# Kernel tuning notes

Hardware: AMD Instinct MI355X
Metric: run time of the kernel (lower is better)

The kernel has to match this reference:

```python
import jax, jax.numpy as jnp
import numpy as np

ROPE_BASE = 10000.0

def _rms_norm(x):
    eps = jnp.asarray(jnp.finfo(x.dtype).eps, x.dtype)
    return x * jax.lax.rsqrt(jnp.mean(x * x, axis=-1, keepdims=True) + eps)

def _rope(x):
    # x: [B, S, H, hd]; rotate-halves variant: y1 = x1*cos + x2*sin, y2 = -x1*sin + x2*cos
    S, hd = x.shape[1], x.shape[3]
    d = hd // 2
    inv_freq = 1.0 / (ROPE_BASE ** (jnp.arange(0, hd, 2, dtype=jnp.float32) / hd))  # [d]
    t = jnp.arange(S, dtype=jnp.float32)
    freqs = jnp.outer(t, inv_freq)                       # [S, d]
    cos = jnp.cos(freqs)[None, :, None, :].astype(x.dtype)
    sin = jnp.sin(freqs)[None, :, None, :].astype(x.dtype)
    x1, x2 = x[..., :d], x[..., d:]
    return jnp.concatenate([x1 * cos + x2 * sin, -x1 * sin + x2 * cos], axis=-1)

def setup_inputs() -> dict:
    key = jax.random.key(0)
    ks = jax.random.split(key, 7)
    B, S, D = 1, 2048, 1024
    std = 0.02
    return {
        "x": jax.random.normal(ks[0], (B, S, D), jnp.float32),
        "v1": jax.random.normal(ks[1], (B, S, D), jnp.float32),
        "Wq": jax.random.normal(ks[2], (D, D), jnp.float32) * std,
        "Wk": jax.random.normal(ks[3], (D, D), jnp.float32) * std,
        "Wv": jax.random.normal(ks[4], (D, D), jnp.float32) * std,
        "Wout": jax.random.normal(ks[5], (D, D), jnp.float32) * std,
        "lambdas": jnp.float32(0.5),
        "n_heads": 16,
    }

def reference(x, v1, Wq, Wk, Wv, Wout, lambdas, n_heads):
    B, S, D = x.shape
    H = n_heads
    hd = D // H
    # QKV projections (CastedLinear, no bias)
    q = (x @ Wq.T).reshape(B, S, H, hd)
    k = (x @ Wk.T).reshape(B, S, H, hd)
    v = (x @ Wv.T).reshape(B, S, H, hd)
    # value residual mix with first-layer values v1
    v = (1.0 - lambdas) * v + lambdas * v1.reshape(B, S, H, hd)
    # per-head RMS norm (no learned scale) then RoPE
    q, k = _rms_norm(q), _rms_norm(k)
    q, k = _rope(q), _rope(k)
    # causal attention (flex_attention default: softmax, scale 1/sqrt(hd))
    scale = 1.0 / jnp.sqrt(jnp.asarray(hd, x.dtype))
    scores = jnp.einsum('bqhd,bkhd->bhqk', q, k) * scale        # [B,H,S,S]
    causal = jnp.tril(jnp.ones((S, S), dtype=bool))
    scores = jnp.where(causal[None, None], scores, jnp.asarray(-jnp.inf, scores.dtype))
    p = jax.nn.softmax(scores, axis=-1)
    y = jnp.einsum('bhqk,bkhd->bqhd', p, v).reshape(B, S, D)
    y = y @ Wout.T
    return (y, v1)
```

## Files before the change

kernel.cpp:

```cpp
#include <hip/hip_runtime.h>
#include <hip/hip_bf16.h>

#define S_LEN 2048
#define D_DIM 1024
#define NH    16
#define NEG_BIG (-1.0e30f)

#define EPI_NORMROPE   1
#define EPI_VMIX_T     2
#define EPI_F32        3
#define EPI_NORMROPE_Q 4
#define EPI_F32A       5

typedef __attribute__((ext_vector_type(8))) short bf16x8;
typedef __attribute__((ext_vector_type(4))) float f32x4;
typedef const __attribute__((address_space(1))) unsigned char gu8_t;
typedef __attribute__((address_space(3))) unsigned char lu8_t;

__device__ __forceinline__ float bf2f(unsigned short h) {
    union { unsigned int u; float f; } v; v.u = ((unsigned int)h) << 16; return v.f;
}
__device__ __forceinline__ unsigned short f2b(float f) {
    union { float f; unsigned int u; } v; v.f = f;
    unsigned int u = v.u;
    return (unsigned short)((u + 0x7FFFu + ((u >> 16) & 1u)) >> 16);
}
__device__ __forceinline__ unsigned short f2b_trunc(float f) {
    union { float f; unsigned int u; } v; v.f = f;
    return (unsigned short)(v.u >> 16);
}

__global__ __launch_bounds__(256)
void to_bf16(const float* __restrict__ x,  const float* __restrict__ wq,
             const float* __restrict__ wk, const float* __restrict__ wv,
             const float* __restrict__ wo,
             unsigned short* __restrict__ xb,  unsigned short* __restrict__ wqb,
             unsigned short* __restrict__ wkb, unsigned short* __restrict__ wvb,
             unsigned short* __restrict__ wob)
{
    const int z = blockIdx.y;
    const float* s; unsigned short* d; int n;
    switch (z) {
        case 0: s = x;  d = xb;  n = S_LEN * D_DIM; break;
        case 1: s = wq; d = wqb; n = D_DIM * D_DIM; break;
        case 2: s = wk; d = wkb; n = D_DIM * D_DIM; break;
        case 3: s = wv; d = wvb; n = D_DIM * D_DIM; break;
        default: s = wo; d = wob; n = D_DIM * D_DIM; break;
    }
    int i8 = blockIdx.x * 256 + threadIdx.x;
    if (i8 * 8 >= n) return;
    const float* sp = s + (size_t)i8 * 8;
    float4 lo = *(const float4*)sp, hi = *(const float4*)(sp + 4);
    uint4 p;
    p.x = f2b(lo.x) | ((unsigned)f2b(lo.y) << 16);
    p.y = f2b(lo.z) | ((unsigned)f2b(lo.w) << 16);
    p.z = f2b(hi.x) | ((unsigned)f2b(hi.y) << 16);
    p.w = f2b(hi.z) | ((unsigned)f2b(hi.w) << 16);
    *(uint4*)(d + (size_t)i8 * 8) = p;
}

__global__ __launch_bounds__(256, 3)
void gemm_bt(const unsigned short* __restrict__ A,
             const unsigned short* __restrict__ B0, const unsigned short* __restrict__ B1,
             const unsigned short* __restrict__ B2,
             void* __restrict__ C0, void* __restrict__ C1, void* __restrict__ C2,
             const float* __restrict__ vmix, const float* __restrict__ lam,
             int epiPack, int splitK)
{
    const int which = blockIdx.z;
    const unsigned short* Bp;
    void* C;
    int epi, kLo, kHi;
    if (splitK) {
        Bp = B0; C = C0; epi = epiPack & 0xff;
        kLo = which * (D_DIM / 2); kHi = kLo + D_DIM / 2;
    } else {
        Bp = (which == 0) ? B0 : ((which == 1) ? B1 : B2);
        C  = (which == 0) ? C0 : ((which == 1) ? C1 : C2);
        epi = (epiPack >> (8 * which)) & 0xff;
        kLo = 0; kHi = D_DIM;
    }
    const int tn = blockIdx.x * 128;
    const int tm = blockIdx.y * 128;

    __shared__ unsigned short Asl[128 * 32];
    __shared__ unsigned short Bsl[128 * 32];

    const int t    = threadIdx.x;
    const int lane = t & 63;
    const int wave = t >> 6;
    const int wm   = (wave >> 1) * 64;
    const int wn   = (wave & 1) * 64;
    const int lrow = lane & 15;
    const int quad = lane >> 4;
    const int srow = lane >> 2;
    const int scol = (lane & 3) * 8;

    f32x4 acc[4][4];
    #pragma unroll
    for (int i = 0; i < 4; ++i)
        #pragma unroll
        for (int j = 0; j < 4; ++j) {
            f32x4 z = {0.f, 0.f, 0.f, 0.f};
            acc[i][j] = z;
        }

    for (int k0 = kLo; k0 < kHi; k0 += 32) {
        #pragma unroll
        for (int rep = 0; rep < 2; ++rep) {
            int grp = wave * 2 + rep;
            int row = grp * 16 + srow;
            __builtin_amdgcn_global_load_lds(
                (gu8_t*)(A + (size_t)(tm + row) * D_DIM + k0 + scol),
                (lu8_t*)&Asl[grp * 512], 16, 0, 0);
            __builtin_amdgcn_global_load_lds(
                (gu8_t*)(Bp + (size_t)(tn + row) * D_DIM + k0 + scol),
                (lu8_t*)&Bsl[grp * 512], 16, 0, 0);
        }
        __syncthreads();
        bf16x8 af[4], bfr[4];
        #pragma unroll
        for (int i = 0; i < 4; ++i)
            af[i] = *(const bf16x8*)(&Asl[(wm + i * 16 + lrow) * 32 + quad * 8]);
        #pragma unroll
        for (int j = 0; j < 4; ++j)
            bfr[j] = *(const bf16x8*)(&Bsl[(wn + j * 16 + lrow) * 32 + quad * 8]);
        #pragma unroll
        for (int i = 0; i < 4; ++i)
            #pragma unroll
            for (int j = 0; j < 4; ++j)
                acc[i][j] = __builtin_amdgcn_mfma_f32_16x16x32_bf16(af[i], bfr[j], acc[i][j], 0, 0, 0);
        __syncthreads();
    }

    if (epi == EPI_NORMROPE || epi == EPI_NORMROPE_Q) {
        const float post = (epi == EPI_NORMROPE_Q) ? 0.18033688011112042f : 1.0f;
        #pragma unroll
        for (int i = 0; i < 4; ++i) {
            #pragma unroll
            for (int r = 0; r < 4; ++r) {
                int row = tm + wm + i * 16 + quad * 4 + r;
                float v0 = acc[i][0][r], v1 = acc[i][1][r];
                float v2 = acc[i][2][r], v3 = acc[i][3][r];
                float ss = v0 * v0 + v1 * v1 + v2 * v2 + v3 * v3;
                ss += __shfl_xor(ss, 1); ss += __shfl_xor(ss, 2);
                ss += __shfl_xor(ss, 4); ss += __shfl_xor(ss, 8);
                float rms = rsqrtf(ss * (1.f / 64.f) + 1.1920929e-7f) * post;
                v0 *= rms; v1 *= rms; v2 *= rms; v3 *= rms;
                float fs = (float)row;
                float a0 = fs * exp2f(-0.41524101186092030f * (float)lrow);
                float a1 = fs * exp2f(-0.41524101186092030f * (float)(16 + lrow));
                float s0, c0, s1, c1;
                __sincosf(a0, &s0, &c0);
                __sincosf(a1, &s1, &c1);
                unsigned short* Cb = (unsigned short*)C;
                size_t base = (size_t)row * D_DIM + tn + wn + lrow;
                Cb[base]      = f2b(v0 * c0 + v2 * s0);
                Cb[base + 16] = f2b(v1 * c1 + v3 * s1);
                Cb[base + 32] = f2b(-v0 * s0 + v2 * c0);
                Cb[base + 48] = f2b(-v1 * s1 + v3 * c1);
            }
        }
    } else if (epi == EPI_VMIX_T) {
        float lamf = *lam;
        #pragma unroll
        for (int i = 0; i < 4; ++i) {
            int cm0 = tm + wm + i * 16 + quad * 4;
            #pragma unroll
            for (int j = 0; j < 4; ++j) {
                int cn = tn + wn + j * 16 + lrow;
                ushort4 pk;
                float vals[4];
                #pragma unroll
                for (int r = 0; r < 4; ++r) {
                    size_t idx = (size_t)(cm0 + r) * D_DIM + cn;
                    vals[r] = (1.f - lamf) * acc[i][j][r] + lamf * vmix[idx];
                }
                pk.x = f2b(vals[0]); pk.y = f2b(vals[1]);
                pk.z = f2b(vals[2]); pk.w = f2b(vals[3]);
                *(ushort4*)((unsigned short*)C + (size_t)cn * S_LEN + cm0) = pk;
            }
        }
    } else if (epi == EPI_F32A) {
        #pragma unroll
        for (int i = 0; i < 4; ++i) {
            int cm0 = tm + wm + i * 16 + quad * 4;
            #pragma unroll
            for (int j = 0; j < 4; ++j) {
                int cn = tn + wn + j * 16 + lrow;
                #pragma unroll
                for (int r = 0; r < 4; ++r)
                    atomicAdd(&((float*)C)[(size_t)(cm0 + r) * D_DIM + cn], acc[i][j][r]);
            }
        }
    } else {
        #pragma unroll
        for (int i = 0; i < 4; ++i) {
            int cm0 = tm + wm + i * 16 + quad * 4;
            #pragma unroll
            for (int j = 0; j < 4; ++j) {
                int cn = tn + wn + j * 16 + lrow;
                #pragma unroll
                for (int r = 0; r < 4; ++r)
                    ((float*)C)[(size_t)(cm0 + r) * D_DIM + cn] = acc[i][j][r];
            }
        }
    }
}

__global__ __launch_bounds__(256, 3)
void attn_mfma(const unsigned short* Qb,
               const unsigned short* __restrict__ Kb,
               const unsigned short* __restrict__ Vtg,
               float* __restrict__ Opart, float* __restrict__ Lpart)
{
    const int bx = blockIdx.x;
    int qt, c;
    if (bx < 32)      { qt = 31 - (bx >> 2);            c = bx & 3;  }
    else if (bx < 56) { int i = bx - 32; qt = 23 - i/3; c = i % 3;   }
    else if (bx < 72) { int i = bx - 56; qt = 15 - (i>>1); c = i & 1;}
    else              { qt = 7 - (bx - 72);             c = 0;       }
    const int jlo = c * 8;
    const int jhi = min(jlo + 7, qt);
    const int h  = blockIdx.y;
    const int t  = threadIdx.x;
    const int w  = t >> 6;
    const int l  = t & 63;
    const int l15  = l & 15;
    const int quad = l >> 4;
    const int hco  = h * 64;
    const int slot = (qt * 4 + c) * NH + h;

    __shared__ unsigned short Ks[2][64][72];
    __shared__ unsigned short Vt[2][64][72];
    __shared__ unsigned short Ps[4][16][72];

    const unsigned short* qrow = Qb + (size_t)(qt * 64 + w * 16 + l15) * D_DIM + hco;
    bf16x8 qf0 = *(const bf16x8*)(qrow + quad * 8);
    bf16x8 qf1 = *(const bf16x8*)(qrow + 32 + quad * 8);

    f32x4 oac[4];
    #pragma unroll
    for (int nt = 0; nt < 4; ++nt) { f32x4 z = {0.f,0.f,0.f,0.f}; oac[nt] = z; }
    float lsum = 0.f;

    const int rr = t >> 2;
    const int dc = (t & 3) * 16;

    const unsigned short* kbase = Kb  + (size_t)rr * D_DIM + hco + dc;
    const unsigned short* vbase = Vtg + (size_t)(hco + rr) * S_LEN + dc;

    uint4 ka0, ka1, va0, va1;
    {
        const unsigned short* kp = kbase + (size_t)jlo * 64 * D_DIM;
        const unsigned short* vp = vbase + (size_t)jlo * 64;
        ka0 = *(const uint4*)kp;  ka1 = *(const uint4*)(kp + 8);
        va0 = *(const uint4*)vp;  va1 = *(const uint4*)(vp + 8);
    }

    const int q_g = qt * 64 + w * 16 + l15;
    const float C2 = -11.541560327111707f;

    for (int j = jlo; j <= jhi; ++j) {
        const int buf = (j - jlo) & 1;
        *(uint4*)&Ks[buf][rr][dc]     = ka0;
        *(uint4*)&Ks[buf][rr][dc + 8] = ka1;
        *(uint4*)&Vt[buf][rr][dc]     = va0;
        *(uint4*)&Vt[buf][rr][dc + 8] = va1;
        __syncthreads();
        if (j < jhi) {
            const unsigned short* kp = kbase + (size_t)(j + 1) * 64 * D_DIM;
            const unsigned short* vp = vbase + (size_t)(j + 1) * 64;
            ka0 = *(const uint4*)kp;  ka1 = *(const uint4*)(kp + 8);
            va0 = *(const uint4*)vp;  va1 = *(const uint4*)(vp + 8);
        }

        f32x4 sac[4];
        #pragma unroll
        for (int nt = 0; nt < 4; ++nt) {
            f32x4 z = {0.f,0.f,0.f,0.f};
            bf16x8 kf0 = *(const bf16x8*)&Ks[buf][nt * 16 + l15][quad * 8];
            z = __builtin_amdgcn_mfma_f32_16x16x32_bf16(kf0, qf0, z, 0, 0, 0);
            bf16x8 kf1 = *(const bf16x8*)&Ks[buf][nt * 16 + l15][32 + quad * 8];
            z = __builtin_amdgcn_mfma_f32_16x16x32_bf16(kf1, qf1, z, 0, 0, 0);
            sac[nt] = z;
        }

        if (j < qt) {
            #pragma unroll
            for (int nt = 0; nt < 4; ++nt) {
                float pe0 = exp2f(sac[nt][0] + C2);
                float pe1 = exp2f(sac[nt][1] + C2);
                float pe2 = exp2f(sac[nt][2] + C2);
                float pe3 = exp2f(sac[nt][3] + C2);
                lsum += (pe0 + pe1) + (pe2 + pe3);
                ushort4 pk;
                pk.x = f2b_trunc(pe0); pk.y = f2b_trunc(pe1);
                pk.z = f2b_trunc(pe2); pk.w = f2b_trunc(pe3);
                *(ushort4*)&Ps[w][l15][nt * 16 + quad * 4] = pk;
            }
        } else {
            #pragma unroll
            for (int nt = 0; nt < 4; ++nt) {
                int key0 = j * 64 + nt * 16 + quad * 4;
                float pe[4];
                #pragma unroll
                for (int r = 0; r < 4; ++r) {
                    float s = sac[nt][r] + C2;
                    if (key0 + r > q_g) s = NEG_BIG;
                    pe[r] = exp2f(s);
                    lsum += pe[r];
                }
                ushort4 pk;
                pk.x = f2b_trunc(pe[0]); pk.y = f2b_trunc(pe[1]);
                pk.z = f2b_trunc(pe[2]); pk.w = f2b_trunc(pe[3]);
                *(ushort4*)&Ps[w][l15][nt * 16 + quad * 4] = pk;
            }
        }

        bf16x8 pf0 = *(const bf16x8*)&Ps[w][l15][quad * 8];
        bf16x8 pf1 = *(const bf16x8*)&Ps[w][l15][32 + quad * 8];
        #pragma unroll
        for (int nt = 0; nt < 4; ++nt) {
            bf16x8 vf0 = *(const bf16x8*)&Vt[buf][nt * 16 + l15][quad * 8];
            oac[nt] = __builtin_amdgcn_mfma_f32_16x16x32_bf16(pf0, vf0, oac[nt], 0, 0, 0);
            bf16x8 vf1 = *(const bf16x8*)&Vt[buf][nt * 16 + l15][32 + quad * 8];
            oac[nt] = __builtin_amdgcn_mfma_f32_16x16x32_bf16(pf1, vf1, oac[nt], 0, 0, 0);
        }
    }

    float lr = lsum;
    lr += __shfl_xor(lr, 16);
    lr += __shfl_xor(lr, 32);
    if (l < 16)
        Lpart[(size_t)slot * 64 + w * 16 + l15] = lr;
    float* Op = Opart + (size_t)slot * 4096;
    #pragma unroll
    for (int nt = 0; nt < 4; ++nt)
        #pragma unroll
        for (int r = 0; r < 4; ++r)
            Op[(size_t)(w * 16 + quad * 4 + r) * 64 + nt * 16 + l15] = oac[nt][r];
}

__global__ __launch_bounds__(256)
void attn_combine(const float* __restrict__ Opart, const float* __restrict__ Lpart,
                  unsigned short* __restrict__ Ob, float* __restrict__ yzero)
{
    const int qt  = blockIdx.x;
    const int h   = blockIdx.y;
    const int t   = threadIdx.x;
    const int row = t >> 2;
    const int c0  = (t & 3) * 16;
    float acc[16];
    #pragma unroll
    for (int i = 0; i < 16; ++i) acc[i] = 0.f;
    float lsum = 0.f;
    for (int c = 0; c < 4; ++c) {
        if (c * 8 > qt) break;
        const size_t slot = (size_t)((qt * 4 + c) * NH + h);
        const float* Op = Opart + slot * 4096 + (size_t)row * 64 + c0;
        #pragma unroll
        for (int g = 0; g < 4; ++g) {
            float4 a = *(const float4*)(Op + g * 4);
            acc[g * 4 + 0] += a.x; acc[g * 4 + 1] += a.y;
            acc[g * 4 + 2] += a.z; acc[g * 4 + 3] += a.w;
        }
        lsum += Lpart[slot * 64 + row];
    }
    const float inv = 1.f / lsum;
    unsigned int pk[8];
    #pragma unroll
    for (int i = 0; i < 8; ++i)
        pk[i] = f2b(acc[2 * i] * inv) | ((unsigned)f2b(acc[2 * i + 1] * inv) << 16);
    unsigned short* dst = Ob + (size_t)(qt * 64 + row) * D_DIM + h * 64 + c0;
    *(uint4*)dst       = make_uint4(pk[0], pk[1], pk[2], pk[3]);
    *(uint4*)(dst + 8) = make_uint4(pk[4], pk[5], pk[6], pk[7]);

    const int flat = (h * 32 + qt) * 256 + t;
    float4 z4 = {0.f, 0.f, 0.f, 0.f};
    float4* yz = (float4*)(yzero + (size_t)flat * 16);
    yz[0] = z4; yz[1] = z4; yz[2] = z4; yz[3] = z4;
}

__global__ __launch_bounds__(256)
void copy_v1(const uint4* __restrict__ src, uint4* __restrict__ dst) {
    int i = blockIdx.x * 256 + threadIdx.x;
    dst[i] = src[i];
}

extern "C" void kernel_launch(void* const* d_in, const int* in_sizes, int n_in,
                              void* d_out, int out_size, void* d_ws, size_t ws_size,
                              hipStream_t stream)
{
    const float* x    = (const float*)d_in[0];
    const float* v1   = (const float*)d_in[1];
    const float* Wq   = (const float*)d_in[2];
    const float* Wk   = (const float*)d_in[3];
    const float* Wv   = (const float*)d_in[4];
    const float* Wout = (const float*)d_in[5];
    const float* lam  = (const float*)d_in[6];
    float* out = (float*)d_out;

    const size_t SD = (size_t)S_LEN * D_DIM;
    const size_t DD = (size_t)D_DIM * D_DIM;
    unsigned short* Qb  = (unsigned short*)d_ws;
    unsigned short* Kb  = Qb + SD;
    unsigned short* Vtg = Kb + SD;
    unsigned short* Ab  = Qb;
    float* Opart = (float*)(Vtg + SD);
    float* Lpart = Opart + (size_t)2048 * 4096;

    unsigned short* Wqb   = (unsigned short*)d_out;
    unsigned short* Wkb   = Wqb + DD;
    unsigned short* Wvb   = Wkb + DD;
    unsigned short* xb    = (unsigned short*)(out + SD);
    unsigned short* Woutb = xb + SD;

    to_bf16<<<dim3(1024, 5), 256, 0, stream>>>(
        x, Wq, Wk, Wv, Wout, xb, Wqb, Wkb, Wvb, Woutb);

    gemm_bt<<<dim3(D_DIM / 128, S_LEN / 128, 3), 256, 0, stream>>>(
        xb, Wqb, Wkb, Wvb, Qb, Kb, Vtg, v1, lam,
        EPI_NORMROPE_Q | (EPI_NORMROPE << 8) | (EPI_VMIX_T << 16), 0);

    attn_mfma<<<dim3(80, NH), 256, 0, stream>>>(Qb, Kb, Vtg, Opart, Lpart);
    attn_combine<<<dim3(S_LEN / 64, NH), 256, 0, stream>>>(Opart, Lpart, Ab, out);

    gemm_bt<<<dim3(D_DIM / 128, S_LEN / 128, 2), 256, 0, stream>>>(
        Ab, Woutb, Woutb, Woutb, d_out, d_out, d_out, nullptr, lam, EPI_F32A, 1);

    copy_v1<<<dim3((unsigned)(SD / 4 / 256)), 256, 0, stream>>>(
        (const uint4*)v1, (uint4*)(out + SD));
}
```

Measured before the change: 178.9 us.

## Use 64x128 tiles for QKV GEMM and raise wave priority around attention MFMAs

Adds a specialized gemm64 kernel with 64-row M tiles for the fused QKV projection, doubling the number of workgroups (768 instead of 384) to fill the CUs better. The output-projection GEMM keeps its 128x128 split-K form but with a slimmer signature. The attention kernel wraps its QK and PV MFMA blocks in s_setprio raises so that waves issuing matrix work get scheduling priority. Smaller tiles reduce per-block data reuse and raise global/LDS traffic per FLOP.

```diff
diff --git a/kernel.cpp b/kernel.cpp
--- a/kernel.cpp
+++ b/kernel.cpp
@@ -60,73 +60,62 @@
 }
 
 __global__ __launch_bounds__(256, 3)
-void gemm_bt(const unsigned short* __restrict__ A,
-             const unsigned short* __restrict__ B0, const unsigned short* __restrict__ B1,
-             const unsigned short* __restrict__ B2,
-             void* __restrict__ C0, void* __restrict__ C1, void* __restrict__ C2,
-             const float* __restrict__ vmix, const float* __restrict__ lam,
-             int epiPack, int splitK)
+void gemm64(const unsigned short* __restrict__ A,
+            const unsigned short* __restrict__ B0, const unsigned short* __restrict__ B1,
+            const unsigned short* __restrict__ B2,
+            void* __restrict__ C0, void* __restrict__ C1, void* __restrict__ C2,
+            const float* __restrict__ vmix, const float* __restrict__ lam,
+            int epiPack)
 {
     const int which = blockIdx.z;
-    const unsigned short* Bp;
-    void* C;
-    int epi, kLo, kHi;
-    if (splitK) {
-        Bp = B0; C = C0; epi = epiPack & 0xff;
-        kLo = which * (D_DIM / 2); kHi = kLo + D_DIM / 2;
-    } else {
-        Bp = (which == 0) ? B0 : ((which == 1) ? B1 : B2);
-        C  = (which == 0) ? C0 : ((which == 1) ? C1 : C2);
-        epi = (epiPack >> (8 * which)) & 0xff;
-        kLo = 0; kHi = D_DIM;
-    }
+    const unsigned short* Bp = (which == 0) ? B0 : ((which == 1) ? B1 : B2);
+    void* C = (which == 0) ? C0 : ((which == 1) ? C1 : C2);
+    const int epi = (epiPack >> (8 * which)) & 0xff;
     const int tn = blockIdx.x * 128;
-    const int tm = blockIdx.y * 128;
-
-    __shared__ unsigned short Asl[128 * 32];
+    const int tm = blockIdx.y * 64;
+
+    __shared__ unsigned short Asl[64 * 32];
     __shared__ unsigned short Bsl[128 * 32];
 
     const int t    = threadIdx.x;
     const int lane = t & 63;
     const int wave = t >> 6;
-    const int wm   = (wave >> 1) * 64;
+    const int wm   = (wave >> 1) * 32;
     const int wn   = (wave & 1) * 64;
     const int lrow = lane & 15;
     const int quad = lane >> 4;
-    const int srow = lane >> 2;
-    const int scol = (lane & 3) * 8;
-
-    f32x4 acc[4][4];
+    const int srow = t >> 2;
+    const int scol = (t & 3) * 8;
+
+    f32x4 acc[2][4];
     #pragma unroll
-    for (int i = 0; i < 4; ++i)
+    for (int i = 0; i < 2; ++i)
         #pragma unroll
         for (int j = 0; j < 4; ++j) {
             f32x4 z = {0.f, 0.f, 0.f, 0.f};
             acc[i][j] = z;
         }
 
-    for (int k0 = kLo; k0 < kHi; k0 += 32) {
-        #pragma unroll
-        for (int rep = 0; rep < 2; ++rep) {
-            int grp = wave * 2 + rep;
-            int row = grp * 16 + srow;
-            __builtin_amdgcn_global_load_lds(
-                (gu8_t*)(A + (size_t)(tm + row) * D_DIM + k0 + scol),
-                (lu8_t*)&Asl[grp * 512], 16, 0, 0);
-            __builtin_amdgcn_global_load_lds(
-                (gu8_t*)(Bp + (size_t)(tn + row) * D_DIM + k0 + scol),
-                (lu8_t*)&Bsl[grp * 512], 16, 0, 0);
-        }
+    for (int k0 = 0; k0 < D_DIM; k0 += 32) {
+        __builtin_amdgcn_global_load_lds(
+            (gu8_t*)(A + (size_t)(tm + srow) * D_DIM + k0 + scol),
+            (lu8_t*)&Asl[t * 8], 16, 0, 0);
+        __builtin_amdgcn_global_load_lds(
+            (gu8_t*)(Bp + (size_t)(tn + srow) * D_DIM + k0 + scol),
+            (lu8_t*)&Bsl[t * 8], 16, 0, 0);
+        __builtin_amdgcn_global_load_lds(
+            (gu8_t*)(Bp + (size_t)(tn + 64 + srow) * D_DIM + k0 + scol),
+            (lu8_t*)&Bsl[2048 + t * 8], 16, 0, 0);
         __syncthreads();
-        bf16x8 af[4], bfr[4];
-        #pragma unroll
-        for (int i = 0; i < 4; ++i)
+        bf16x8 af[2], bfr[4];
+        #pragma unroll
+        for (int i = 0; i < 2; ++i)
             af[i] = *(const bf16x8*)(&Asl[(wm + i * 16 + lrow) * 32 + quad * 8]);
         #pragma unroll
         for (int j = 0; j < 4; ++j)
             bfr[j] = *(const bf16x8*)(&Bsl[(wn + j * 16 + lrow) * 32 + quad * 8]);
         #pragma unroll
-        for (int i = 0; i < 4; ++i)
+        for (int i = 0; i < 2; ++i)
             #pragma unroll
             for (int j = 0; j < 4; ++j)
                 acc[i][j] = __builtin_amdgcn_mfma_f32_16x16x32_bf16(af[i], bfr[j], acc[i][j], 0, 0, 0);
@@ -136,7 +125,7 @@
     if (epi == EPI_NORMROPE || epi == EPI_NORMROPE_Q) {
         const float post = (epi == EPI_NORMROPE_Q) ? 0.18033688011112042f : 1.0f;
         #pragma unroll
-        for (int i = 0; i < 4; ++i) {
+        for (int i = 0; i < 2; ++i) {
             #pragma unroll
             for (int r = 0; r < 4; ++r) {
                 int row = tm + wm + i * 16 + quad * 4 + r;
@@ -164,7 +153,7 @@
     } else if (epi == EPI_VMIX_T) {
         float lamf = *lam;
         #pragma unroll
-        for (int i = 0; i < 4; ++i) {
+        for (int i = 0; i < 2; ++i) {
             int cm0 = tm + wm + i * 16 + quad * 4;
             #pragma unroll
             for (int j = 0; j < 4; ++j) {
@@ -181,7 +170,87 @@
                 *(ushort4*)((unsigned short*)C + (size_t)cn * S_LEN + cm0) = pk;
             }
         }
-    } else if (epi == EPI_F32A) {
+    } else {
+        #pragma unroll
+        for (int i = 0; i < 2; ++i) {
+            int cm0 = tm + wm + i * 16 + quad * 4;
+            #pragma unroll
+            for (int j = 0; j < 4; ++j) {
+                int cn = tn + wn + j * 16 + lrow;
+                #pragma unroll
+                for (int r = 0; r < 4; ++r)
+                    ((float*)C)[(size_t)(cm0 + r) * D_DIM + cn] = acc[i][j][r];
+            }
+        }
+    }
+}
+
+__global__ __launch_bounds__(256, 3)
+void gemm_bt(const unsigned short* __restrict__ A,
+             const unsigned short* __restrict__ B0,
+             void* __restrict__ C0,
+             const float* __restrict__ lam,
+             int epi, int splitK)
+{
+    const int which = blockIdx.z;
+    const unsigned short* Bp = B0;
+    void* C = C0;
+    int kLo = 0, kHi = D_DIM;
+    if (splitK) { kLo = which * (D_DIM / 2); kHi = kLo + D_DIM / 2; }
+    const int tn = blockIdx.x * 128;
+    const int tm = blockIdx.y * 128;
+
+    __shared__ unsigned short Asl[128 * 32];
+    __shared__ unsigned short Bsl[128 * 32];
+
+    const int t    = threadIdx.x;
+    const int lane = t & 63;
+    const int wave = t >> 6;
+    const int wm   = (wave >> 1) * 64;
+    const int wn   = (wave & 1) * 64;
+    const int lrow = lane & 15;
+    const int quad = lane >> 4;
+    const int srow = lane >> 2;
+    const int scol = (lane & 3) * 8;
+
+    f32x4 acc[4][4];
+    #pragma unroll
+    for (int i = 0; i < 4; ++i)
+        #pragma unroll
+        for (int j = 0; j < 4; ++j) {
+            f32x4 z = {0.f, 0.f, 0.f, 0.f};
+            acc[i][j] = z;
+        }
+
+    for (int k0 = kLo; k0 < kHi; k0 += 32) {
+        #pragma unroll
+        for (int rep = 0; rep < 2; ++rep) {
+            int grp = wave * 2 + rep;
+            int row = grp * 16 + srow;
+            __builtin_amdgcn_global_load_lds(
+                (gu8_t*)(A + (size_t)(tm + row) * D_DIM + k0 + scol),
+                (lu8_t*)&Asl[grp * 512], 16, 0, 0);
+            __builtin_amdgcn_global_load_lds(
+                (gu8_t*)(Bp + (size_t)(tn + row) * D_DIM + k0 + scol),
+                (lu8_t*)&Bsl[grp * 512], 16, 0, 0);
+        }
+        __syncthreads();
+        bf16x8 af[4], bfr[4];
+        #pragma unroll
+        for (int i = 0; i < 4; ++i)
+            af[i] = *(const bf16x8*)(&Asl[(wm + i * 16 + lrow) * 32 + quad * 8]);
+        #pragma unroll
+        for (int j = 0; j < 4; ++j)
+            bfr[j] = *(const bf16x8*)(&Bsl[(wn + j * 16 + lrow) * 32 + quad * 8]);
+        #pragma unroll
+        for (int i = 0; i < 4; ++i)
+            #pragma unroll
+            for (int j = 0; j < 4; ++j)
+                acc[i][j] = __builtin_amdgcn_mfma_f32_16x16x32_bf16(af[i], bfr[j], acc[i][j], 0, 0, 0);
+        __syncthreads();
+    }
+
+    if (epi == EPI_F32A) {
         #pragma unroll
         for (int i = 0; i < 4; ++i) {
             int cm0 = tm + wm + i * 16 + quad * 4;
@@ -276,6 +345,7 @@
         }
 
         f32x4 sac[4];
+        __builtin_amdgcn_s_setprio(1);
         #pragma unroll
         for (int nt = 0; nt < 4; ++nt) {
             f32x4 z = {0.f,0.f,0.f,0.f};
@@ -285,6 +355,7 @@
             z = __builtin_amdgcn_mfma_f32_16x16x32_bf16(kf1, qf1, z, 0, 0, 0);
             sac[nt] = z;
         }
+        __builtin_amdgcn_s_setprio(0);
 
         if (j < qt) {
             #pragma unroll
@@ -320,6 +391,7 @@
 
         bf16x8 pf0 = *(const bf16x8*)&Ps[w][l15][quad * 8];
         bf16x8 pf1 = *(const bf16x8*)&Ps[w][l15][32 + quad * 8];
+        __builtin_amdgcn_s_setprio(1);
         #pragma unroll
         for (int nt = 0; nt < 4; ++nt) {
             bf16x8 vf0 = *(const bf16x8*)&Vt[buf][nt * 16 + l15][quad * 8];
@@ -327,6 +399,7 @@
             bf16x8 vf1 = *(const bf16x8*)&Vt[buf][nt * 16 + l15][32 + quad * 8];
             oac[nt] = __builtin_amdgcn_mfma_f32_16x16x32_bf16(pf1, vf1, oac[nt], 0, 0, 0);
         }
+        __builtin_amdgcn_s_setprio(0);
     }
 
     float lr = lsum;
@@ -419,15 +492,15 @@
     to_bf16<<<dim3(1024, 5), 256, 0, stream>>>(
         x, Wq, Wk, Wv, Wout, xb, Wqb, Wkb, Wvb, Woutb);
 
-    gemm_bt<<<dim3(D_DIM / 128, S_LEN / 128, 3), 256, 0, stream>>>(
+    gemm64<<<dim3(D_DIM / 128, S_LEN / 64, 3), 256, 0, stream>>>(
         xb, Wqb, Wkb, Wvb, Qb, Kb, Vtg, v1, lam,
-        EPI_NORMROPE_Q | (EPI_NORMROPE << 8) | (EPI_VMIX_T << 16), 0);
+        EPI_NORMROPE_Q | (EPI_NORMROPE << 8) | (EPI_VMIX_T << 16));
 
     attn_mfma<<<dim3(80, NH), 256, 0, stream>>>(Qb, Kb, Vtg, Opart, Lpart);
     attn_combine<<<dim3(S_LEN / 64, NH), 256, 0, stream>>>(Opart, Lpart, Ab, out);
 
     gemm_bt<<<dim3(D_DIM / 128, S_LEN / 128, 2), 256, 0, stream>>>(
-        Ab, Woutb, Woutb, Woutb, d_out, d_out, d_out, nullptr, lam, EPI_F32A, 1);
+        Ab, Woutb, d_out, lam, EPI_F32A, 1);
 
     copy_v1<<<dim3((unsigned)(SD / 4 / 256)), 256, 0, stream>>>(
         (const uint4*)v1, (uint4*)(out + SD));
```

After: 176.0 us. About the same (-1.6%).
